# Optimization experiments

Measured on AMD Instinct MI355X. Metric: run time of the kernel, lower is better.

Reference implementation:

```python
import jax, jax.numpy as jnp
import numpy as np

N_HEAD = 16
HEAD_DIM = 64
ROPE_BASE = 10000.0


def _rope_cos_sin(T, dim, dtype):
    inv_freq = 1.0 / (ROPE_BASE ** (np.arange(0, dim, 2, dtype=np.float32) / dim))
    t = np.arange(T, dtype=np.float32)
    freqs = np.outer(t, inv_freq)              # [T, dim/2]
    emb = np.concatenate([freqs, freqs], -1)   # [T, dim]
    return jnp.asarray(np.cos(emb), dtype), jnp.asarray(np.sin(emb), dtype)


def _rotate_half(x):
    x1, x2 = x[..., : x.shape[-1] // 2], x[..., x.shape[-1] // 2 :]
    return jnp.concatenate([-x2, x1], axis=-1)


def setup_inputs() -> dict:
    key = jax.random.key(0)
    k1, k2, k3 = jax.random.split(key, 3)
    B, T, C = 4, 2048, 1024
    x = jax.random.normal(k1, (B, T, C), jnp.float32)
    w_qkv = jax.random.normal(k2, (C, 3 * C), jnp.float32) * (C ** -0.5)
    w_proj = jax.random.normal(k3, (C, C), jnp.float32) * (C ** -0.5)
    return {"x": x, "w_qkv": w_qkv, "w_proj": w_proj}


def reference(x, w_qkv, w_proj):
    B, T, C = x.shape
    H, D = N_HEAD, HEAD_DIM
    qkv = x @ w_qkv                                   # [B, T, 3C]
    q, k, v = jnp.split(qkv, 3, axis=-1)
    # [B, H, T, D]
    q = q.reshape(B, T, H, D).transpose(0, 2, 1, 3)
    k = k.reshape(B, T, H, D).transpose(0, 2, 1, 3)
    v = v.reshape(B, T, H, D).transpose(0, 2, 1, 3)
    cos, sin = _rope_cos_sin(T, D, x.dtype)           # [T, D]
    q = q * cos + _rotate_half(q) * sin
    k = k * cos + _rotate_half(k) * sin
    scale = D ** -0.5
    scores = jnp.einsum("bhqd,bhkd->bhqk", q, k) * scale
    causal = jnp.tril(jnp.ones((T, T), bool))
    scores = jnp.where(causal, scores, jnp.finfo(scores.dtype).min)
    attn = jax.nn.softmax(scores, axis=-1)
    y = jnp.einsum("bhqk,bhkd->bhqd", attn, v)        # [B, H, T, D]
    y = y.transpose(0, 2, 1, 3).reshape(B, T, C)
    return y @ w_proj
```

## Files before the change

### kernel.cpp

```cpp
#include <hip/hip_runtime.h>
#include <cstdint>

typedef unsigned short u16;
typedef __attribute__((ext_vector_type(4))) float f32x4;
typedef __attribute__((ext_vector_type(4))) unsigned short u16x4;
typedef __attribute__((ext_vector_type(8))) unsigned short u16x8;
typedef __attribute__((ext_vector_type(8))) __bf16 bf16x8;

#define DEV __device__ __forceinline__

DEV u16 f2bf(float f) {
  union { float f; uint32_t u; } x{f};
  uint32_t r = (x.u + 0x7fffu + ((x.u >> 16) & 1u)) >> 16;
  return (u16)r;
}

DEV void gl_lds16(const void* g, void* l) {
  __builtin_amdgcn_global_load_lds((__attribute__((address_space(1))) void*)(g),
                                   (__attribute__((address_space(3))) void*)(l),
                                   16, 0, 0);
}

__global__ __launch_bounds__(256) void prep(const float* __restrict__ x, u16* __restrict__ xb,
                                            const float* __restrict__ wqkv, u16* __restrict__ wqkvT,
                                            const float* __restrict__ wproj, u16* __restrict__ wprojT) {
  const int bid = blockIdx.x, tid = threadIdx.x;
  if (bid < 8192) {
    int i = bid * 256 + tid;
    float4 v = ((const float4*)x)[i];
    u16x4 o = { f2bf(v.x), f2bf(v.y), f2bf(v.z), f2bf(v.w) };
    ((u16x4*)xb)[i] = o;
    return;
  }
  __shared__ float tile[64][65];
  const float* in; u16* out; int R, C, bx, by;
  if (bid < 8960) {
    int idx = bid - 8192; in = wqkv;  out = wqkvT;  R = 1024; C = 3072; bx = idx % 48; by = idx / 48;
  } else {
    int idx = bid - 8960; in = wproj; out = wprojT; R = 1024; C = 1024; bx = idx & 15; by = idx >> 4;
  }
  const int c0 = bx * 64, r0 = by * 64;
  const int tx = tid & 63, ty = tid >> 6;
  for (int r = ty; r < 64; r += 4) tile[r][tx] = in[(size_t)(r0 + r) * C + c0 + tx];
  __syncthreads();
  for (int r = ty; r < 64; r += 4) out[(size_t)(c0 + r) * R + r0 + tx] = f2bf(tile[tx][r]);
}

template <int EPI>
__global__ __launch_bounds__(256) void gemm_bt(const u16* __restrict__ A,
                                               const u16* __restrict__ Bt,
                                               u16* __restrict__ qo, u16* __restrict__ ko,
                                               u16* __restrict__ vo, float* __restrict__ outf) {
  extern __shared__ char lds_occupancy_pad[];
  const int K = 1024;
  __shared__ __align__(16) u16 As[128 * 64];
  __shared__ __align__(16) u16 Bs[128 * 64];
  const int m0 = blockIdx.y * 128, n0 = blockIdx.x * 128;
  const int tid = threadIdx.x;
  const int w = tid >> 6, lane = tid & 63, quad = lane >> 4, l15 = lane & 15;
  const int mw = (w >> 1) * 64, nw = (w & 1) * 64;

  const int srow = tid >> 3;
  const int schunk = ((tid & 7) ^ (srow & 7)) * 8;

  f32x4 acc[4][4];
#pragma unroll
  for (int i = 0; i < 4; ++i)
#pragma unroll
    for (int j = 0; j < 4; ++j) acc[i][j] = f32x4{0.f, 0.f, 0.f, 0.f};

  const u16* ga0 = A + (size_t)(m0 + srow) * K + schunk;
  const u16* gb0 = Bt + (size_t)(n0 + srow) * K + schunk;

  const int sw7 = l15 & 7;
  int aoff[4], boff[4];
#pragma unroll
  for (int i = 0; i < 4; ++i) aoff[i] = (mw + i * 16 + l15) * 64;
#pragma unroll
  for (int j = 0; j < 4; ++j) boff[j] = (nw + j * 16 + l15) * 64;
  int coff[2];
#pragma unroll
  for (int kk = 0; kk < 2; ++kk) coff[kk] = ((kk * 4 + quad) ^ sw7) * 8;

  for (int k0 = 0; k0 < K; k0 += 64) {
#pragma unroll
    for (int ss = 0; ss < 4; ++ss) {
      gl_lds16(ga0 + (size_t)ss * 32 * K + k0, As + ss * 2048 + tid * 8);
      gl_lds16(gb0 + (size_t)ss * 32 * K + k0, Bs + ss * 2048 + tid * 8);
    }
    __syncthreads();
#pragma unroll
    for (int kk = 0; kk < 2; ++kk) {
      bf16x8 af[4], bfv[4];
#pragma unroll
      for (int i = 0; i < 4; ++i) af[i] = *(const bf16x8*)(As + aoff[i] + coff[kk]);
#pragma unroll
      for (int j = 0; j < 4; ++j) bfv[j] = *(const bf16x8*)(Bs + boff[j] + coff[kk]);
#pragma unroll
      for (int i = 0; i < 4; ++i)
#pragma unroll
        for (int j = 0; j < 4; ++j)
          acc[i][j] = __builtin_amdgcn_mfma_f32_16x16x32_bf16(af[i], bfv[j], acc[i][j], 0, 0, 0);
    }
    __syncthreads();
  }

  if (EPI == 1) {
#pragma unroll
    for (int i = 0; i < 4; ++i)
#pragma unroll
      for (int j = 0; j < 4; ++j)
#pragma unroll
        for (int r = 0; r < 4; ++r) {
          int row = m0 + mw + i * 16 + quad * 4 + r;
          int col = n0 + nw + j * 16 + l15;
          outf[(size_t)row * 1024 + col] = acc[i][j][r];
        }
    return;
  }
  const int s = n0 >> 10;
  if (s == 2) {
    u16* tile = (w & 1) ? Bs : As;
#pragma unroll
    for (int j = 0; j < 4; ++j) {
      const int d = j * 16 + l15;
      const int swz = l15 * 8;
#pragma unroll
      for (int i = 0; i < 4; ++i)
#pragma unroll
        for (int r = 0; r < 4; ++r) {
          int tl = mw + i * 16 + quad * 4 + r;
          tile[d * 128 + (tl ^ swz)] = f2bf(acc[i][j][r]);
        }
    }
    __syncthreads();
    const int b = m0 >> 11, t0g = m0 & 2047;
    const int hh0 = (n0 & 1023) >> 6;
    const int tch = tid & 15;
#pragma unroll
    for (int p = 0; p < 8; ++p) {
      int row = (tid >> 4) + p * 16;
      int d = row & 63, head = row >> 6;
      const u16* src = head ? Bs : As;
      u16x8 v = *(const u16x8*)(src + d * 128 + ((tch * 8) ^ ((d & 15) * 8)));
      *(u16x8*)(vo + ((size_t)((b * 16 + hh0 + head) * 64 + d)) * 2048 + t0g + tch * 8) = v;
    }
  } else {
    const int hh = ((n0 & 1023) + nw) >> 6;
    u16* dst = (s == 0) ? qo : ko;
    const float QS = (s == 0) ? 0.18033688011112042f : 1.0f;
    const float C1 = -0.4152410118609203f;
    const float R2PI = 0.15915494309189535f;
    const float inv0 = __builtin_amdgcn_exp2f((float)l15 * C1) * R2PI;
    const float inv1 = __builtin_amdgcn_exp2f((float)(16 + l15) * C1) * R2PI;
#pragma unroll
    for (int i = 0; i < 4; ++i)
#pragma unroll
      for (int r = 0; r < 4; ++r) {
        int row = m0 + mw + i * 16 + quad * 4 + r;
        int b = row >> 11, t = row & 2047;
        size_t base = ((size_t)(b * 16 + hh) * 2048 + t) * 64;
        float tf = (float)t;
        float a0 = tf * inv0; a0 -= floorf(a0);
        float a1 = tf * inv1; a1 -= floorf(a1);
        float c0 = __builtin_amdgcn_cosf(a0), s0 = __builtin_amdgcn_sinf(a0);
        float c1 = __builtin_amdgcn_cosf(a1), s1 = __builtin_amdgcn_sinf(a1);
        float x0 = acc[i][0][r], y0 = acc[i][2][r];
        float x1 = acc[i][1][r], y1 = acc[i][3][r];
        dst[base + l15]      = f2bf((x0 * c0 - y0 * s0) * QS);
        dst[base + 32 + l15] = f2bf((y0 * c0 + x0 * s0) * QS);
        dst[base + 16 + l15] = f2bf((x1 * c1 - y1 * s1) * QS);
        dst[base + 48 + l15] = f2bf((y1 * c1 + x1 * s1) * QS);
      }
  }
}

__global__ __launch_bounds__(256) void attn_kernel(const u16* __restrict__ q,
                                                   const u16* __restrict__ k,
                                                   const u16* __restrict__ vt,
                                                   u16* __restrict__ y) {
  const int T = 2048;
  const int bh = blockIdx.x;
  const int qi = 15 - blockIdx.y;
  const int q0 = qi * 128;
  const int tid = threadIdx.x;
  const int w = tid >> 6, lane = tid & 63, quad = lane >> 4, l15 = lane & 15;
  __shared__ __align__(16) u16 Ks[64 * 64];
  __shared__ __align__(16) u16 Vs[64 * 64];
  __shared__ __align__(16) u16 Pq[4 * 32 * 72];
  u16* Pw = Pq + w * 32 * 72;

  const int sw = l15 & 7;
  int koff[4][2], voff[4][2];
#pragma unroll
  for (int kf = 0; kf < 4; ++kf) {
    koff[kf][0] = (kf * 16 + l15) * 64 + ((quad ^ sw) * 8);
    koff[kf][1] = (kf * 16 + l15) * 64 + (((quad + 4) ^ sw) * 8);
  }
#pragma unroll
  for (int df = 0; df < 4; ++df) {
    voff[df][0] = (df * 16 + l15) * 64 + ((quad ^ sw) * 8);
    voff[df][1] = (df * 16 + l15) * 64 + (((quad + 4) ^ sw) * 8);
  }
  const int pwoff = l15 * 72 + quad * 4;
  const int proff = l15 * 72 + quad * 8;

  const int r_ = tid >> 3, c_ = tid & 7, ssw = r_ & 7;
  const u16* kg = k + (size_t)bh * T * 64;
  const u16* vg = vt + (size_t)bh * 64 * T;
  const int sk0 = r_ * 64 + (c_ ^ ssw) * 8;
  const int sk1 = (r_ + 32) * 64 + (c_ ^ ssw) * 8;
  const int sv0 = r_ * T + (c_ ^ ssw) * 8;
  const int sv1 = (r_ + 32) * T + (c_ ^ ssw) * 8;

  const int b_ = bh >> 4, h_ = bh & 15;
  const int q0w = q0 + w * 32;

  bf16x8 qf_[2][2];
#pragma unroll
  for (int qf = 0; qf < 2; ++qf)
#pragma unroll
    for (int h = 0; h < 2; ++h)
      qf_[qf][h] = *(const bf16x8*)(q + ((size_t)bh * T + q0w + qf * 16 + l15) * 64 + h * 32 + quad * 8);

  f32x4 o[2][4];
  float li[2] = {0.f, 0.f};
#pragma unroll
  for (int qf = 0; qf < 2; ++qf)
#pragma unroll
    for (int df = 0; df < 4; ++df) o[qf][df] = f32x4{0.f, 0.f, 0.f, 0.f};

  const int nit = 2 * qi + 2;

  for (int it = 0; it < nit; ++it) {
    const int kb = it * 64;
    gl_lds16(kg + (size_t)kb * 64 + sk0, Ks + tid * 8);
    gl_lds16(kg + (size_t)kb * 64 + sk1, Ks + 2048 + tid * 8);
    gl_lds16(vg + kb + sv0, Vs + tid * 8);
    gl_lds16(vg + kb + sv1, Vs + 2048 + tid * 8);
    __syncthreads();

    bf16x8 ka[4][2];
#pragma unroll
    for (int kf = 0; kf < 4; ++kf) {
      ka[kf][0] = *(const bf16x8*)(Ks + koff[kf][0]);
      ka[kf][1] = *(const bf16x8*)(Ks + koff[kf][1]);
    }
    f32x4 st[2][4];
    __builtin_amdgcn_s_setprio(1);
#pragma unroll
    for (int kf = 0; kf < 4; ++kf)
#pragma unroll
      for (int qf = 0; qf < 2; ++qf) {
        f32x4 s = f32x4{0.f, 0.f, 0.f, 0.f};
        s = __builtin_amdgcn_mfma_f32_16x16x32_bf16(ka[kf][0], qf_[qf][0], s, 0, 0, 0);
        s = __builtin_amdgcn_mfma_f32_16x16x32_bf16(ka[kf][1], qf_[qf][1], s, 0, 0, 0);
        st[qf][kf] = s;
      }
    __builtin_amdgcn_s_setprio(0);

    if (it >= nit - 2) {
#pragma unroll
      for (int qf = 0; qf < 2; ++qf) {
        const int qrow = q0w + qf * 16 + l15;
#pragma unroll
        for (int kf = 0; kf < 4; ++kf)
#pragma unroll
          for (int r = 0; r < 4; ++r)
            if (kb + kf * 16 + quad * 4 + r > qrow) st[qf][kf][r] = -__builtin_inff();
      }
    }

#pragma unroll
    for (int qf = 0; qf < 2; ++qf) {
      float rs = 0.f;
#pragma unroll
      for (int kf = 0; kf < 4; ++kf) {
        float p0 = __builtin_amdgcn_exp2f(st[qf][kf][0]);
        float p1 = __builtin_amdgcn_exp2f(st[qf][kf][1]);
        float p2 = __builtin_amdgcn_exp2f(st[qf][kf][2]);
        float p3 = __builtin_amdgcn_exp2f(st[qf][kf][3]);
        rs += (p0 + p1) + (p2 + p3);
        union { float f; uint32_t u; } u0{p0}, u1{p1}, u2{p2}, u3{p3};
        uint32_t pk01 = __builtin_amdgcn_perm(u1.u + 0x8000u, u0.u + 0x8000u, 0x07060302u);
        uint32_t pk23 = __builtin_amdgcn_perm(u3.u + 0x8000u, u2.u + 0x8000u, 0x07060302u);
        uint2 pk; pk.x = pk01; pk.y = pk23;
        *(uint2*)(Pw + qf * 16 * 72 + pwoff + kf * 16) = pk;
      }
      li[qf] += rs;
    }

#pragma unroll
    for (int qf = 0; qf < 2; ++qf) {
      bf16x8 pb0 = *(const bf16x8*)(Pw + qf * 16 * 72 + proff);
      bf16x8 pb1 = *(const bf16x8*)(Pw + qf * 16 * 72 + proff + 32);
      __builtin_amdgcn_s_setprio(1);
#pragma unroll
      for (int df = 0; df < 4; ++df) {
        bf16x8 va0 = *(const bf16x8*)(Vs + voff[df][0]);
        bf16x8 va1 = *(const bf16x8*)(Vs + voff[df][1]);
        o[qf][df] = __builtin_amdgcn_mfma_f32_16x16x32_bf16(va0, pb0, o[qf][df], 0, 0, 0);
        o[qf][df] = __builtin_amdgcn_mfma_f32_16x16x32_bf16(va1, pb1, o[qf][df], 0, 0, 0);
      }
      __builtin_amdgcn_s_setprio(0);
    }
    __syncthreads();
  }

#pragma unroll
  for (int qf = 0; qf < 2; ++qf) {
    float l = li[qf];
    l += __shfl_xor(l, 16, 64);
    l += __shfl_xor(l, 32, 64);
    const float inv = 1.f / l;
    const size_t base = ((size_t)b_ * 2048 + q0w + qf * 16 + l15) * 1024 + h_ * 64;
#pragma unroll
    for (int df = 0; df < 4; ++df) {
      u16x4 ov;
#pragma unroll
      for (int r = 0; r < 4; ++r) ov[r] = f2bf(o[qf][df][r] * inv);
      *(u16x4*)(y + base + df * 16 + quad * 4) = ov;
    }
  }
}

extern "C" void kernel_launch(void* const* d_in, const int* in_sizes, int n_in,
                              void* d_out, int out_size, void* d_ws, size_t ws_size,
                              hipStream_t stream) {
  const float* x = (const float*)d_in[0];
  const float* w_qkv = (const float*)d_in[1];
  const float* w_proj = (const float*)d_in[2];
  float* out = (float*)d_out;

  u16* xb = (u16*)d_ws;
  u16* wqkvT = xb + 8388608;
  u16* wprojT = wqkvT + 3145728;
  u16* qb = wprojT + 1048576;
  u16* kbuf = qb + 8388608;
  u16* vtb = kbuf + 8388608;
  u16* yb = xb;

  prep<<<9216, 256, 0, stream>>>(x, xb, w_qkv, wqkvT, w_proj, wprojT);
  gemm_bt<0><<<dim3(24, 64), 256, 21504, stream>>>(xb, wqkvT, qb, kbuf, vtb, nullptr);
  attn_kernel<<<dim3(64, 16), 256, 0, stream>>>(qb, kbuf, vtb, yb);
  gemm_bt<1><<<dim3(8, 64), 256, 0, stream>>>(yb, wprojT, nullptr, nullptr, nullptr, out);
}
```

Measured before the change: 233.1 us.

## Add 256x256-tile pipelined QKV GEMM with double-buffered LDS and interleaved barriers

Replaces the 128x128 QKV projection GEMM with a dedicated 512-thread kernel that computes 256x256 output tiles, double-buffers A and B tiles in LDS via direct global-to-LDS loads, and interleaves staging with MFMA groups under raw s_barrier and explicit vmcnt waits. It also remaps block indices so neighbouring blocks share A/B panels, and raises MFMA wave priority. The goal is more operand reuse per LDS byte and better overlap of memory with compute. The cost is 64KB of LDS per block and heavy register pressure from 32 accumulators per thread, plus reliance on hand-counted vmcnt ordering that could be fragile.

```diff
diff --git a/kernel.cpp b/kernel.cpp
--- a/kernel.cpp
+++ b/kernel.cpp
@@ -20,6 +20,8 @@
                                    (__attribute__((address_space(3))) void*)(l),
                                    16, 0, 0);
 }
+
+DEV void bar() { asm volatile("s_barrier" ::: "memory"); }
 
 __global__ __launch_bounds__(256) void prep(const float* __restrict__ x, u16* __restrict__ xb,
                                             const float* __restrict__ wqkv, u16* __restrict__ wqkvT,
@@ -44,6 +46,204 @@
   for (int r = ty; r < 64; r += 4) tile[r][tx] = in[(size_t)(r0 + r) * C + c0 + tx];
   __syncthreads();
   for (int r = ty; r < 64; r += 4) out[(size_t)(c0 + r) * R + r0 + tx] = f2bf(tile[tx][r]);
+}
+
+__global__ __launch_bounds__(512, 2) void gemm256_qkv(const u16* __restrict__ A,
+                                                      const u16* __restrict__ Bt,
+                                                      u16* __restrict__ qo,
+                                                      u16* __restrict__ ko,
+                                                      u16* __restrict__ vo) {
+  __shared__ __align__(16) u16 Ls[4][16384];
+  u16* const As0 = Ls[0]; u16* const As1 = Ls[1];
+  u16* const Bs0 = Ls[2]; u16* const Bs1 = Ls[3];
+
+  const int lin = blockIdx.x;
+  const int id = (lin & 7) * 48 + (lin >> 3);
+  const int bx = id % 12, by = id / 12;
+  const int m0 = by * 256, n0 = bx * 256;
+  const int tid = threadIdx.x;
+  const int w = tid >> 6, lane = tid & 63, quad = lane >> 4, l15 = lane & 15;
+  const int wm = w >> 2, wn = w & 3;
+
+  const int rd0 = tid >> 3;
+  const int sch = ((tid & 7) ^ (rd0 & 7)) * 8;
+
+  const u16* gA = A + (size_t)m0 * 1024;
+  const u16* gB = Bt + (size_t)n0 * 1024;
+
+  const int sw = l15 & 7;
+  int coff[2];
+#pragma unroll
+  for (int kk = 0; kk < 2; ++kk) coff[kk] = ((kk * 4 + quad) ^ sw) * 8;
+  const int abase = l15 * 64;
+  const int bbase = ((wn & 1) * 64 + l15) * 64;
+  const u16* Ah0 = As0 + wm * 8192;
+  const u16* Ah1 = As1 + wm * 8192;
+  const u16* Bh0 = Bs0 + (wn >> 1) * 8192;
+  const u16* Bh1 = Bs1 + (wn >> 1) * 8192;
+
+  f32x4 acc[8][4];
+#pragma unroll
+  for (int i = 0; i < 8; ++i)
+#pragma unroll
+    for (int j = 0; j < 4; ++j) acc[i][j] = f32x4{0.f, 0.f, 0.f, 0.f};
+
+  auto stage = [&](const u16* p, u16* l) {
+    gl_lds16(p + (size_t)rd0 * 1024 + sch, l + tid * 8);
+    gl_lds16(p + (size_t)(rd0 + 64) * 1024 + sch, l + 4096 + tid * 8);
+  };
+
+  auto mma8 = [&](bf16x8 (&af)[4][2], bf16x8 (&bf2)[2][2], int mo, int no) {
+    __builtin_amdgcn_s_setprio(1);
+#pragma unroll
+    for (int mf = 0; mf < 4; ++mf)
+#pragma unroll
+      for (int nf = 0; nf < 2; ++nf)
+#pragma unroll
+        for (int kk = 0; kk < 2; ++kk)
+          acc[mo + mf][no + nf] = __builtin_amdgcn_mfma_f32_16x16x32_bf16(
+              af[mf][kk], bf2[nf][kk], acc[mo + mf][no + nf], 0, 0, 0);
+    __builtin_amdgcn_s_setprio(0);
+  };
+
+  stage(gA, As0);
+  stage(gA + 131072, As0 + 8192);
+  stage(gB, Bs0);
+  stage(gB + 131072, Bs0 + 8192);
+  stage(gB + 64, Bs1);
+  stage(gB + 64 + 131072, Bs1 + 8192);
+  asm volatile("s_waitcnt vmcnt(0)" ::: "memory");
+  bar();
+
+  for (int m = 0; m < 8; ++m) {
+    const bool st = (m < 7);
+    const u16* gA1 = gA + m * 128 + 64;
+    const u16* gA2 = gA + m * 128 + 128;
+    const u16* gB2 = gB + m * 128 + 128;
+    const u16* gB3 = gB + m * 128 + 192;
+    bf16x8 af[4][2], b0f[2][2], b1f[2][2];
+
+#pragma unroll
+    for (int mf = 0; mf < 4; ++mf)
+#pragma unroll
+      for (int kk = 0; kk < 2; ++kk)
+        af[mf][kk] = *(const bf16x8*)(Ah0 + abase + mf * 1024 + coff[kk]);
+#pragma unroll
+    for (int nf = 0; nf < 2; ++nf)
+#pragma unroll
+      for (int kk = 0; kk < 2; ++kk)
+        b0f[nf][kk] = *(const bf16x8*)(Bh0 + bbase + nf * 1024 + coff[kk]);
+    stage(gA1, As1);
+    bar(); mma8(af, b0f, 0, 0); bar();
+#pragma unroll
+    for (int nf = 0; nf < 2; ++nf)
+#pragma unroll
+      for (int kk = 0; kk < 2; ++kk)
+        b1f[nf][kk] = *(const bf16x8*)(Bh0 + bbase + (2 + nf) * 1024 + coff[kk]);
+    stage(gA1 + 131072, As1 + 8192);
+    bar(); mma8(af, b1f, 0, 2); bar();
+#pragma unroll
+    for (int mf = 0; mf < 4; ++mf)
+#pragma unroll
+      for (int kk = 0; kk < 2; ++kk)
+        af[mf][kk] = *(const bf16x8*)(Ah0 + abase + (4 + mf) * 1024 + coff[kk]);
+    if (st) stage(gB2, Bs0);
+    bar(); mma8(af, b1f, 4, 2); bar();
+    if (st) stage(gB2 + 131072, Bs0 + 8192);
+    bar(); mma8(af, b0f, 4, 0);
+    if (st) asm volatile("s_waitcnt vmcnt(4)" ::: "memory");
+    else    asm volatile("s_waitcnt vmcnt(0)" ::: "memory");
+    bar();
+
+#pragma unroll
+    for (int mf = 0; mf < 4; ++mf)
+#pragma unroll
+      for (int kk = 0; kk < 2; ++kk)
+        af[mf][kk] = *(const bf16x8*)(Ah1 + abase + mf * 1024 + coff[kk]);
+#pragma unroll
+    for (int nf = 0; nf < 2; ++nf)
+#pragma unroll
+      for (int kk = 0; kk < 2; ++kk)
+        b0f[nf][kk] = *(const bf16x8*)(Bh1 + bbase + nf * 1024 + coff[kk]);
+    if (st) stage(gA2, As0);
+    bar(); mma8(af, b0f, 0, 0); bar();
+#pragma unroll
+    for (int nf = 0; nf < 2; ++nf)
+#pragma unroll
+      for (int kk = 0; kk < 2; ++kk)
+        b1f[nf][kk] = *(const bf16x8*)(Bh1 + bbase + (2 + nf) * 1024 + coff[kk]);
+    if (st) stage(gA2 + 131072, As0 + 8192);
+    bar(); mma8(af, b1f, 0, 2); bar();
+#pragma unroll
+    for (int mf = 0; mf < 4; ++mf)
+#pragma unroll
+      for (int kk = 0; kk < 2; ++kk)
+        af[mf][kk] = *(const bf16x8*)(Ah1 + abase + (4 + mf) * 1024 + coff[kk]);
+    if (st) stage(gB3, Bs1);
+    bar(); mma8(af, b1f, 4, 2); bar();
+    if (st) stage(gB3 + 131072, Bs1 + 8192);
+    bar(); mma8(af, b0f, 4, 0);
+    if (st) asm volatile("s_waitcnt vmcnt(4)" ::: "memory");
+    else    asm volatile("s_waitcnt vmcnt(0)" ::: "memory");
+    bar();
+  }
+
+  const int s = n0 >> 10;
+  if (s == 2) {
+    u16* VT = &Ls[0][0];
+    __syncthreads();
+#pragma unroll
+    for (int nf = 0; nf < 4; ++nf) {
+      const int d = wn * 64 + nf * 16 + l15;
+      const int swz = (d & 15) * 8;
+#pragma unroll
+      for (int mf = 0; mf < 8; ++mf)
+#pragma unroll
+        for (int r = 0; r < 4; ++r) {
+          int t = wm * 128 + mf * 16 + quad * 4 + r;
+          VT[d * 256 + (t ^ swz)] = f2bf(acc[mf][nf][r]);
+        }
+    }
+    __syncthreads();
+    const int b = m0 >> 11, t0g = m0 & 2047;
+    const int hh0 = (n0 & 1023) >> 6;
+    const int tch = tid & 31;
+#pragma unroll
+    for (int p = 0; p < 16; ++p) {
+      int row = (tid >> 5) + p * 16;
+      u16x8 v = *(const u16x8*)(VT + row * 256 + ((tch * 8) ^ ((row & 15) * 8)));
+      *(u16x8*)(vo + ((size_t)((b * 16 + hh0 + (row >> 6)) * 64 + (row & 63))) * 2048 +
+                t0g + tch * 8) = v;
+    }
+  } else {
+    u16* dst = (s == 0) ? qo : ko;
+    const float QS = (s == 0) ? 0.18033688011112042f : 1.0f;
+    const float C1 = -0.4152410118609203f;
+    const float R2PI = 0.15915494309189535f;
+    const int hh = ((n0 & 1023) >> 6) + wn;
+    const int rowbase = m0 + wm * 128 + quad * 4;
+    const float inv0 = __builtin_amdgcn_exp2f((float)l15 * C1) * R2PI;
+    const float inv1 = __builtin_amdgcn_exp2f((float)(16 + l15) * C1) * R2PI;
+#pragma unroll
+    for (int mf = 0; mf < 8; ++mf)
+#pragma unroll
+      for (int r = 0; r < 4; ++r) {
+        int row = rowbase + mf * 16 + r;
+        int b = row >> 11, t = row & 2047;
+        size_t base = ((size_t)(b * 16 + hh) * 2048 + t) * 64;
+        float tf = (float)t;
+        float a0 = tf * inv0; a0 -= floorf(a0);
+        float a1 = tf * inv1; a1 -= floorf(a1);
+        float c0 = __builtin_amdgcn_cosf(a0), s0 = __builtin_amdgcn_sinf(a0);
+        float c1 = __builtin_amdgcn_cosf(a1), s1 = __builtin_amdgcn_sinf(a1);
+        float x0 = acc[mf][0][r], y0 = acc[mf][2][r];
+        float x1 = acc[mf][1][r], y1 = acc[mf][3][r];
+        dst[base + l15]      = f2bf((x0 * c0 - y0 * s0) * QS);
+        dst[base + 32 + l15] = f2bf((y0 * c0 + x0 * s0) * QS);
+        dst[base + 16 + l15] = f2bf((x1 * c1 - y1 * s1) * QS);
+        dst[base + 48 + l15] = f2bf((y1 * c1 + x1 * s1) * QS);
+      }
+  }
 }
 
 template <int EPI>
@@ -117,61 +317,6 @@
           outf[(size_t)row * 1024 + col] = acc[i][j][r];
         }
     return;
-  }
-  const int s = n0 >> 10;
-  if (s == 2) {
-    u16* tile = (w & 1) ? Bs : As;
-#pragma unroll
-    for (int j = 0; j < 4; ++j) {
-      const int d = j * 16 + l15;
-      const int swz = l15 * 8;
-#pragma unroll
-      for (int i = 0; i < 4; ++i)
-#pragma unroll
-        for (int r = 0; r < 4; ++r) {
-          int tl = mw + i * 16 + quad * 4 + r;
-          tile[d * 128 + (tl ^ swz)] = f2bf(acc[i][j][r]);
-        }
-    }
-    __syncthreads();
-    const int b = m0 >> 11, t0g = m0 & 2047;
-    const int hh0 = (n0 & 1023) >> 6;
-    const int tch = tid & 15;
-#pragma unroll
-    for (int p = 0; p < 8; ++p) {
-      int row = (tid >> 4) + p * 16;
-      int d = row & 63, head = row >> 6;
-      const u16* src = head ? Bs : As;
-      u16x8 v = *(const u16x8*)(src + d * 128 + ((tch * 8) ^ ((d & 15) * 8)));
-      *(u16x8*)(vo + ((size_t)((b * 16 + hh0 + head) * 64 + d)) * 2048 + t0g + tch * 8) = v;
-    }
-  } else {
-    const int hh = ((n0 & 1023) + nw) >> 6;
-    u16* dst = (s == 0) ? qo : ko;
-    const float QS = (s == 0) ? 0.18033688011112042f : 1.0f;
-    const float C1 = -0.4152410118609203f;
-    const float R2PI = 0.15915494309189535f;
-    const float inv0 = __builtin_amdgcn_exp2f((float)l15 * C1) * R2PI;
-    const float inv1 = __builtin_amdgcn_exp2f((float)(16 + l15) * C1) * R2PI;
-#pragma unroll
-    for (int i = 0; i < 4; ++i)
-#pragma unroll
-      for (int r = 0; r < 4; ++r) {
-        int row = m0 + mw + i * 16 + quad * 4 + r;
-        int b = row >> 11, t = row & 2047;
-        size_t base = ((size_t)(b * 16 + hh) * 2048 + t) * 64;
-        float tf = (float)t;
-        float a0 = tf * inv0; a0 -= floorf(a0);
-        float a1 = tf * inv1; a1 -= floorf(a1);
-        float c0 = __builtin_amdgcn_cosf(a0), s0 = __builtin_amdgcn_sinf(a0);
-        float c1 = __builtin_amdgcn_cosf(a1), s1 = __builtin_amdgcn_sinf(a1);
-        float x0 = acc[i][0][r], y0 = acc[i][2][r];
-        float x1 = acc[i][1][r], y1 = acc[i][3][r];
-        dst[base + l15]      = f2bf((x0 * c0 - y0 * s0) * QS);
-        dst[base + 32 + l15] = f2bf((y0 * c0 + x0 * s0) * QS);
-        dst[base + 16 + l15] = f2bf((x1 * c1 - y1 * s1) * QS);
-        dst[base + 48 + l15] = f2bf((y1 * c1 + x1 * s1) * QS);
-      }
   }
 }
 
@@ -341,7 +486,7 @@
   u16* yb = xb;
 
   prep<<<9216, 256, 0, stream>>>(x, xb, w_qkv, wqkvT, w_proj, wprojT);
-  gemm_bt<0><<<dim3(24, 64), 256, 21504, stream>>>(xb, wqkvT, qb, kbuf, vtb, nullptr);
+  gemm256_qkv<<<384, 512, 0, stream>>>(xb, wqkvT, qb, kbuf, vtb);
   attn_kernel<<<dim3(64, 16), 256, 0, stream>>>(qb, kbuf, vtb, yb);
   gemm_bt<1><<<dim3(8, 64), 256, 0, stream>>>(yb, wprojT, nullptr, nullptr, nullptr, out);
 }
```

Result: no change. 234.4 us (+0.6%).
